# Optimization experiments

Measured on AMD Instinct MI355X. Metric: run time of the kernel, lower is better.

The kernel has to match this reference:

```python
import jax, jax.numpy as jnp
import numpy as np

B, N, DIM = 4, 1024, 2048
H, HKV, D = 16, 4, 128          # n_heads, n_kv_heads, head_dim
CACHE = 3072                     # cached KV length
WINDOW = 2048                    # max_window_len (sliding window)
EPS = 1e-6


def setup_inputs() -> dict:
    key = jax.random.key(0)
    ks = jax.random.split(key, 10)
    x = jax.random.normal(ks[0], (B, N, DIM), dtype=jnp.float32)
    past_k = jax.random.normal(ks[1], (B, HKV, CACHE, D), dtype=jnp.float32)
    past_v = jax.random.normal(ks[2], (B, HKV, CACHE, D), dtype=jnp.float32)
    # RoPE angles for the current segment (absolute positions CACHE..CACHE+N-1),
    # matching MultiLevelRoPE 'face' level: freqs = 1/theta**(arange(0,D,2)/D)
    pos = jnp.arange(CACHE, CACHE + N, dtype=jnp.float32)
    inv_freq = 1.0 / (10000.0 ** (jnp.arange(0, D, 2, dtype=jnp.float32) / D))
    ang = pos[:, None] * inv_freq[None, :]          # [N, D//2]
    freqs_cos = jnp.cos(ang)
    freqs_sin = jnp.sin(ang)
    s = 0.02
    Wq = jax.random.normal(ks[3], (H * D, DIM), dtype=jnp.float32) * s
    Wk = jax.random.normal(ks[4], (HKV * D, DIM), dtype=jnp.float32) * s
    Wv = jax.random.normal(ks[5], (HKV * D, DIM), dtype=jnp.float32) * s
    Wo = jax.random.normal(ks[6], (DIM, H * D), dtype=jnp.float32) * s
    bo = jnp.zeros((DIM,), dtype=jnp.float32)
    wq_norm = jnp.ones((D,), dtype=jnp.float32)
    wk_norm = jnp.ones((D,), dtype=jnp.float32)
    return {"x": x, "past_k": past_k, "past_v": past_v,
            "freqs_cos": freqs_cos, "freqs_sin": freqs_sin,
            "Wq": Wq, "Wk": Wk, "Wv": Wv, "Wo": Wo, "bo": bo,
            "wq_norm": wq_norm, "wk_norm": wk_norm}


def _rms_norm(t, w):
    # torch.nn.RMSNorm over head_dim
    return t * jax.lax.rsqrt(jnp.mean(t * t, axis=-1, keepdims=True) + EPS) * w


def _rope(t, cos, sin):
    # interleaved-pair complex rotation, as in MultiLevelRoPE.apply
    # t: [B, h, N, D]; cos/sin: [N, D//2]
    t2 = t.reshape(*t.shape[:-1], D // 2, 2)
    x0, x1 = t2[..., 0], t2[..., 1]
    c = cos[None, None, :, :]
    s = sin[None, None, :, :]
    r0 = x0 * c - x1 * s
    r1 = x0 * s + x1 * c
    return jnp.stack([r0, r1], axis=-1).reshape(t.shape)


def reference(x, past_k, past_v, freqs_cos, freqs_sin,
              Wq, Wk, Wv, Wo, bo, wq_norm, wk_norm):
    # projections -> [B, h, N, D]
    q = (x @ Wq.T).reshape(B, N, H, D).transpose(0, 2, 1, 3)
    k = (x @ Wk.T).reshape(B, N, HKV, D).transpose(0, 2, 1, 3)
    v = (x @ Wv.T).reshape(B, N, HKV, D).transpose(0, 2, 1, 3)
    # qk rms_norm on head_dim
    q = _rms_norm(q, wq_norm)
    k = _rms_norm(k, wk_norm)
    # RoPE on current segment (cached K already rotated)
    q = _rope(q, freqs_cos, freqs_sin)
    k = _rope(k, freqs_cos, freqs_sin)
    # append to cache -> M = CACHE + N
    k_all = jnp.concatenate([past_k, k], axis=2)   # [B, HKV, M, D]
    v_all = jnp.concatenate([past_v, v], axis=2)
    # repeat_kv for GQA
    n_rep = H // HKV
    k_rep = jnp.repeat(k_all, n_rep, axis=1)       # [B, H, M, D]
    v_rep = jnp.repeat(v_all, n_rep, axis=1)
    M = CACHE + N
    scale = 1.0 / jnp.sqrt(jnp.asarray(D, dtype=q.dtype))
    scores = jnp.einsum('bhnd,bhmd->bhnm', q, k_rep) * scale
    # causal + sliding-window mask over absolute positions
    qpos = jnp.arange(N) + CACHE                   # [N]
    kpos = jnp.arange(M)                           # [M]
    allowed = (kpos[None, :] <= qpos[:, None]) & (qpos[:, None] - kpos[None, :] < WINDOW)
    scores = jnp.where(allowed[None, None], scores, jnp.asarray(-1e30, dtype=scores.dtype))
    probs = jax.nn.softmax(scores, axis=-1)
    attn = jnp.einsum('bhnm,bhmd->bhnd', probs, v_rep)
    attn = attn.transpose(0, 2, 1, 3).reshape(B, N, H * D)
    return attn @ Wo.T + bo
```

## Files before the change

### kernel.cpp

```cpp
#include <hip/hip_runtime.h>
#include <hip/hip_bf16.h>
#include <stdint.h>

typedef unsigned short u16;
typedef unsigned int u32;
typedef __attribute__((ext_vector_type(8))) __bf16 bfrag;
typedef __attribute__((ext_vector_type(4))) float f32x4;
typedef __attribute__((ext_vector_type(4))) unsigned short u16x4;

__device__ __forceinline__ u16 f2bf(float f){
  union { float f; u32 u; } v; v.f = f;
  u32 u = v.u;
  return (u16)((u + 0x7fffu + ((u >> 16) & 1u)) >> 16);
}

__device__ __forceinline__ void gload_lds16(const void* g, void* l){
  __builtin_amdgcn_global_load_lds(
      (__attribute__((address_space(1))) void*)(unsigned long long)g,
      (__attribute__((address_space(3))) void*)(u32)(unsigned long long)l,
      16, 0, 0);
}

__global__ void __launch_bounds__(256) k_cvt(const float* __restrict__ s, u16* __restrict__ d, int n4){
  int i = blockIdx.x*256 + threadIdx.x;
  if (i >= n4) return;
  float4 v = ((const float4*)s)[i];
  u16x4 o; o[0]=f2bf(v.x); o[1]=f2bf(v.y); o[2]=f2bf(v.z); o[3]=f2bf(v.w);
  ((u16x4*)d)[i] = o;
}

__global__ void __launch_bounds__(256) k_cvt_past(const float* __restrict__ s, u16* __restrict__ d, int n4){
  int i = blockIdx.x*256 + threadIdx.x;
  if (i >= n4) return;
  int e = i*4;
  int row = e >> 7;
  int col = e & 127;
  int bh = row / 3072;
  int m = row - bh*3072;
  float4 v = ((const float4*)s)[i];
  u16x4 o; o[0]=f2bf(v.x); o[1]=f2bf(v.y); o[2]=f2bf(v.z); o[3]=f2bf(v.w);
  *(u16x4*)(d + ((size_t)(bh*4096 + m) << 7) + col) = o;
}

template<int EPI>
__global__ void __launch_bounds__(256) k_gemm(
    const u16* __restrict__ A, const u16* __restrict__ Bm,
    u16* __restrict__ Cb, float* __restrict__ Cf, const float* __restrict__ bias,
    int M, int Nn, int K)
{
  __shared__ u16 lsA[2][4096];
  __shared__ u16 lsB[2][4096];
  const int t = threadIdx.x, lane = t & 63, wid = t >> 6;
  const int l15 = lane & 15, l4 = lane >> 4;
  const int wm = wid >> 1, wn = wid & 1;
  const int bn = blockIdx.x, bm = blockIdx.y;
  const u16* Ab = A + (size_t)bm*128*K;
  const u16* Bb = Bm + (size_t)bn*128*K;

  auto stage = [&](u16* ls, const u16* g, int kof){
    #pragma unroll
    for (int r = 0; r < 2; ++r){
      int row = r*64 + (t >> 2);
      int s = (t & 3) ^ ((row >> 1) & 3);
      gload_lds16(g + (size_t)row*K + kof + s*8, ls + r*2048 + wid*512);
    }
  };

  f32x4 acc[4][4] = {};
  stage(&lsA[0][0], Ab, 0);
  stage(&lsB[0][0], Bb, 0);
  const int NT = K >> 5;
  const int sl = l4 ^ ((l15 >> 1) & 3);
  const int ra0 = wm*64 + l15, rb0 = wn*64 + l15;
  for (int kt = 0; kt < NT; ++kt){
    __syncthreads();
    const int cur = kt & 1;
    if (kt + 1 < NT){
      stage(&lsA[cur ^ 1][0], Ab, (kt + 1)*32);
      stage(&lsB[cur ^ 1][0], Bb, (kt + 1)*32);
    }
    bfrag af[4], bfv[4];
    #pragma unroll
    for (int i = 0; i < 4; ++i){
      af[i]  = *(const bfrag*)&lsA[cur][(ra0 + i*16)*32 + sl*8];
      bfv[i] = *(const bfrag*)&lsB[cur][(rb0 + i*16)*32 + sl*8];
    }
    #pragma unroll
    for (int i = 0; i < 4; ++i)
      #pragma unroll
      for (int j = 0; j < 4; ++j)
        acc[i][j] = __builtin_amdgcn_mfma_f32_16x16x32_bf16(af[i], bfv[j], acc[i][j], 0, 0, 0);
  }
  const int row0 = bm*128 + wm*64, col0 = bn*128 + wn*64;
  #pragma unroll
  for (int i = 0; i < 4; ++i)
    #pragma unroll
    for (int j = 0; j < 4; ++j){
      int cc = col0 + j*16 + l15;
      float bv = (EPI == 1) ? bias[cc] : 0.f;
      #pragma unroll
      for (int r = 0; r < 4; ++r){
        int rr = row0 + i*16 + l4*4 + r;
        if (EPI == 0) Cb[(size_t)rr*Nn + cc] = f2bf(acc[i][j][r]);
        else          Cf[(size_t)rr*Nn + cc] = acc[i][j][r] + bv;
      }
    }
}

__global__ void __launch_bounds__(256) k_rmsrope(
    const u16* __restrict__ proj, const float* __restrict__ cosb, const float* __restrict__ sinb,
    const float* __restrict__ wq, const float* __restrict__ wk,
    u16* __restrict__ q_ro, u16* __restrict__ k_all, u16* __restrict__ v_all)
{
  const int bn = blockIdx.x;
  const int b = bn >> 10, n = bn & 1023;
  const int lane = threadIdx.x & 63, w = threadIdx.x >> 6;
  const int chunk = blockIdx.y*4 + w;
  const u16* src = proj + (size_t)bn*3072 + chunk*128 + lane*2;
  const u32 raw = *(const u32*)src;
  union { u32 u; float f; } a, c2;
  a.u = raw << 16; c2.u = raw & 0xffff0000u;
  float x0 = a.f, x1 = c2.f;
  if (chunk >= 20){
    int hk = chunk - 20;
    *(u32*)(v_all + (((size_t)(b*4 + hk)*4096 + 3072 + n) << 7) + lane*2) = raw;
    return;
  }
  float ss = x0*x0 + x1*x1;
  #pragma unroll
  for (int m = 1; m < 64; m <<= 1) ss += __shfl_xor(ss, m, 64);
  float inv = rsqrtf(ss*(1.f/128.f) + 1e-6f);
  const float* wn2 = (chunk < 16) ? wq : wk;
  x0 *= inv*wn2[lane*2]; x1 *= inv*wn2[lane*2 + 1];
  float cz = cosb[n*64 + lane], sz = sinb[n*64 + lane];
  float r0 = x0*cz - x1*sz;
  float r1 = x0*sz + x1*cz;
  u32 outp = (u32)f2bf(r0) | ((u32)f2bf(r1) << 16);
  if (chunk < 16){
    *(u32*)(q_ro + (((size_t)(b*16 + chunk)*1024 + n) << 7) + lane*2) = outp;
  } else {
    int hk = chunk - 16;
    *(u32*)(k_all + (((size_t)(b*4 + hk)*4096 + 3072 + n) << 7) + lane*2) = outp;
  }
}

__global__ void __launch_bounds__(256) k_transpose_v(const u16* __restrict__ v_all, u16* __restrict__ v_t){
  __shared__ u16 T[64][65];
  const int mt = blockIdx.x, dt = blockIdx.y, pl = blockIdx.z;
  const u16* src = v_all + (size_t)pl*4096*128 + (size_t)mt*64*128 + dt*64;
  u16* dst = v_t + (size_t)pl*128*4096 + (size_t)dt*64*4096 + mt*64;
  const int t = threadIdx.x;
  #pragma unroll
  for (int r = 0; r < 2; ++r){
    int row = r*32 + (t >> 3);
    int c8 = (t & 7)*8;
    bfrag v = *(const bfrag*)(src + (size_t)row*128 + c8);
    union { bfrag v; u16 e[8]; } uv; uv.v = v;
    #pragma unroll
    for (int j = 0; j < 8; ++j) T[row][c8 + j] = uv.e[j];
  }
  __syncthreads();
  #pragma unroll
  for (int r = 0; r < 2; ++r){
    int drow = r*32 + (t >> 3);
    int m8 = (t & 7)*8;
    union { bfrag v; u16 e[8]; } uv;
    #pragma unroll
    for (int j = 0; j < 8; ++j) uv.e[j] = T[m8 + j][drow];
    *(bfrag*)(dst + (size_t)drow*4096 + m8) = uv.v;
  }
}

__global__ void __launch_bounds__(512) k_attn(
    const u16* __restrict__ q_ro, const u16* __restrict__ k_all,
    const u16* __restrict__ v_t, u16* __restrict__ attn_o)
{
  __shared__ u16 Kl[2][64*128];
  __shared__ u16 Vt[2][128*64];
  const int bid = blockIdx.x;
  const int qt = bid & 15, hk = (bid >> 4) & 3, b = bid >> 6;
  const int t = threadIdx.x, lane = t & 63, w = t >> 6;
  const int l15 = lane & 15, l4 = lane >> 4;
  const int h = hk*4 + (w >> 1);
  const int qbase = qt*64 + (w & 1)*32;

  const u16* qplane = q_ro + (size_t)(b*16 + h)*1024*128;
  const u16* kplane = k_all + (size_t)(b*4 + hk)*4096*128;
  const u16* vplane = v_t  + (size_t)(b*4 + hk)*128*4096;

  bfrag qf[2][4];
  #pragma unroll
  for (int qmi = 0; qmi < 2; ++qmi){
    const u16* qrow = qplane + (size_t)(qbase + qmi*16 + l15)*128;
    #pragma unroll
    for (int dks = 0; dks < 4; ++dks)
      qf[qmi][dks] = *(const bfrag*)(qrow + dks*32 + l4*8);
  }

  const int kb0 = qt*64 + 1024;
  auto stage = [&](int buf, int kb){
    #pragma unroll
    for (int r = 0; r < 2; ++r){
      int row = r*32 + (t >> 4);
      int s = (t & 15) ^ (row & 7);
      gload_lds16(kplane + (size_t)(kb + row)*128 + s*8, &Kl[buf][r*4096 + w*512]);
    }
    #pragma unroll
    for (int r = 0; r < 2; ++r){
      int row = r*64 + (t >> 3);
      int s = (t & 7) ^ (row & 7);
      gload_lds16(vplane + (size_t)row*4096 + kb + s*8, &Vt[buf][r*4096 + w*512]);
    }
  };

  f32x4 acc_o[8][2] = {};
  float m_run[2] = {-1e30f, -1e30f};
  float l_run[2] = {0.f, 0.f};
  const int qpos0 = 3072 + qbase + l15;
  const int qpmin = 3072 + qbase;
  const float sc = 0.08838834764831845f;

  stage(0, kb0);
  int cur = 0;
  for (int c = 0; c < 33; ++c){
    __syncthreads();
    const int kb = kb0 + c*64;
    if (c < 32) stage(cur ^ 1, kb + 64);

    f32x4 acc_s[4][2] = {};
    #pragma unroll
    for (int dks = 0; dks < 4; ++dks){
      bfrag kf[4];
      #pragma unroll
      for (int kni = 0; kni < 4; ++kni){
        int rk = kni*16 + l15;
        int slot = (dks*4 + l4) ^ (rk & 7);
        kf[kni] = *(const bfrag*)&Kl[cur][rk*128 + slot*8];
      }
      #pragma unroll
      for (int kni = 0; kni < 4; ++kni)
        #pragma unroll
        for (int qmi = 0; qmi < 2; ++qmi)
          acc_s[kni][qmi] = __builtin_amdgcn_mfma_f32_16x16x32_bf16(kf[kni], qf[qmi][dks], acc_s[kni][qmi], 0, 0, 0);
    }

    const bool full = (kb >= qpmin - 2016) && (kb + 63 <= qpmin);
    #pragma unroll
    for (int kni = 0; kni < 4; ++kni)
      #pragma unroll
      for (int qmi = 0; qmi < 2; ++qmi)
        #pragma unroll
        for (int r = 0; r < 4; ++r){
          float s = acc_s[kni][qmi][r]*sc;
          if (!full){
            int kpos = kb + kni*16 + l4*4 + r;
            int dq = (qpos0 + qmi*16) - kpos;
            if (dq < 0 || dq >= 2048) s = -__builtin_inff();
          }
          acc_s[kni][qmi][r] = s;
        }

    float ef[2];
    #pragma unroll
    for (int qmi = 0; qmi < 2; ++qmi){
      float mx = -__builtin_inff();
      #pragma unroll
      for (int kni = 0; kni < 4; ++kni)
        #pragma unroll
        for (int r = 0; r < 4; ++r) mx = fmaxf(mx, acc_s[kni][qmi][r]);
      mx = fmaxf(mx, __shfl_xor(mx, 16, 64));
      mx = fmaxf(mx, __shfl_xor(mx, 32, 64));
      float mnew = fmaxf(m_run[qmi], mx);
      ef[qmi] = __expf(m_run[qmi] - mnew);
      float ls = 0.f;
      #pragma unroll
      for (int kni = 0; kni < 4; ++kni)
        #pragma unroll
        for (int r = 0; r < 4; ++r){
          float p = __expf(acc_s[kni][qmi][r] - mnew);
          acc_s[kni][qmi][r] = p;
          ls += p;
        }
      ls += __shfl_xor(ls, 16, 64);
      ls += __shfl_xor(ls, 32, 64);
      l_run[qmi] = l_run[qmi]*ef[qmi] + ls;
      m_run[qmi] = mnew;
    }

    #pragma unroll
    for (int dj = 0; dj < 8; ++dj)
      #pragma unroll
      for (int qmi = 0; qmi < 2; ++qmi)
        #pragma unroll
        for (int r = 0; r < 4; ++r) acc_o[dj][qmi][r] *= ef[qmi];

    u32 pk[4][2][2];
    #pragma unroll
    for (int kni = 0; kni < 4; ++kni)
      #pragma unroll
      for (int qmi = 0; qmi < 2; ++qmi){
        pk[kni][qmi][0] = (u32)f2bf(acc_s[kni][qmi][0]) | ((u32)f2bf(acc_s[kni][qmi][1]) << 16);
        pk[kni][qmi][1] = (u32)f2bf(acc_s[kni][qmi][2]) | ((u32)f2bf(acc_s[kni][qmi][3]) << 16);
      }

    const int srcA = ((l4 & 1) << 5) + l15;
    const int srcB = srcA + 16;
    const bool hi = (l4 >> 1) != 0;
    #pragma unroll
    for (int ks = 0; ks < 2; ++ks){
      bfrag vf[8];
      #pragma unroll
      for (int dj = 0; dj < 8; ++dj){
        int rd = dj*16 + l15;
        int slot = (ks*4 + l4) ^ (rd & 7);
        vf[dj] = *(const bfrag*)&Vt[cur][rd*64 + slot*8];
      }
      #pragma unroll
      for (int qmi = 0; qmi < 2; ++qmi){
        u32 a0 = (u32)__shfl((int)pk[ks*2][qmi][0], srcA, 64);
        u32 a1 = (u32)__shfl((int)pk[ks*2][qmi][1], srcA, 64);
        u32 b0 = (u32)__shfl((int)pk[ks*2][qmi][0], srcB, 64);
        u32 b1 = (u32)__shfl((int)pk[ks*2][qmi][1], srcB, 64);
        u32 c0 = (u32)__shfl((int)pk[ks*2+1][qmi][0], srcA, 64);
        u32 c1 = (u32)__shfl((int)pk[ks*2+1][qmi][1], srcA, 64);
        u32 d0 = (u32)__shfl((int)pk[ks*2+1][qmi][0], srcB, 64);
        u32 d1 = (u32)__shfl((int)pk[ks*2+1][qmi][1], srcB, 64);
        union { u32 u[4]; bfrag v; } pf;
        pf.u[0] = hi ? c0 : a0;
        pf.u[1] = hi ? c1 : a1;
        pf.u[2] = hi ? d0 : b0;
        pf.u[3] = hi ? d1 : b1;
        #pragma unroll
        for (int dj = 0; dj < 8; ++dj)
          acc_o[dj][qmi] = __builtin_amdgcn_mfma_f32_16x16x32_bf16(vf[dj], pf.v, acc_o[dj][qmi], 0, 0, 0);
      }
    }
    cur ^= 1;
  }

  #pragma unroll
  for (int qmi = 0; qmi < 2; ++qmi){
    float inv = 1.0f / l_run[qmi];
    int bn = b*1024 + qbase + qmi*16 + l15;
    u16* orow = attn_o + (size_t)bn*2048 + h*128;
    #pragma unroll
    for (int dj = 0; dj < 8; ++dj){
      u16x4 o;
      #pragma unroll
      for (int r = 0; r < 4; ++r) o[r] = f2bf(acc_o[dj][qmi][r]*inv);
      *(u16x4*)(orow + dj*16 + l4*4) = o;
    }
  }
}

extern "C" void kernel_launch(void* const* d_in, const int* in_sizes, int n_in,
                              void* d_out, int out_size, void* d_ws, size_t ws_size,
                              hipStream_t stream)
{
  const float* x      = (const float*)d_in[0];
  const float* past_k = (const float*)d_in[1];
  const float* past_v = (const float*)d_in[2];
  const float* fcos   = (const float*)d_in[3];
  const float* fsin   = (const float*)d_in[4];
  const float* Wq     = (const float*)d_in[5];
  const float* Wk     = (const float*)d_in[6];
  const float* Wv     = (const float*)d_in[7];
  const float* Wo     = (const float*)d_in[8];
  const float* bo     = (const float*)d_in[9];
  const float* wqn    = (const float*)d_in[10];
  const float* wkn    = (const float*)d_in[11];
  float* out = (float*)d_out;
  char* ws = (char*)d_ws;

  u16* xb    = (u16*)(ws);
  u16* wqkv  = (u16*)(ws + 16777216);
  u16* wo_b  = (u16*)(ws + 29360128);
  u16* q_ro  = (u16*)(ws + 37748736);
  u16* k_all = (u16*)(ws + 54525952);
  u16* v_all = (u16*)(ws + 71303168);
  u16* v_t   = (u16*)(ws + 88080384);
  u16* proj  = (u16*)(ws + 104857600);
  u16* attn_o = proj;

  k_cvt<<<8192, 256, 0, stream>>>(x, xb, 2097152);
  k_cvt<<<4096, 256, 0, stream>>>(Wq, wqkv, 1048576);
  k_cvt<<<1024, 256, 0, stream>>>(Wk, wqkv + 2048*2048, 262144);
  k_cvt<<<1024, 256, 0, stream>>>(Wv, wqkv + 2560*2048, 262144);
  k_cvt<<<4096, 256, 0, stream>>>(Wo, wo_b, 1048576);
  k_cvt_past<<<6144, 256, 0, stream>>>(past_k, k_all, 1572864);
  k_cvt_past<<<6144, 256, 0, stream>>>(past_v, v_all, 1572864);

  k_gemm<0><<<dim3(24, 32), 256, 0, stream>>>(xb, wqkv, proj, nullptr, nullptr, 4096, 3072, 2048);
  k_rmsrope<<<dim3(4096, 6), 256, 0, stream>>>(proj, fcos, fsin, wqn, wkn, q_ro, k_all, v_all);
  k_transpose_v<<<dim3(64, 2, 16), 256, 0, stream>>>(v_all, v_t);
  k_attn<<<256, 512, 0, stream>>>(q_ro, k_all, v_t, attn_o);
  k_gemm<1><<<dim3(16, 32), 256, 0, stream>>>(attn_o, wo_b, nullptr, out, bo, 4096, 2048, 2048);
}
```

Before: 285.5 us.

## Rewrite attention with 32x32 MFMA, lazy rescale, and fuse past-V conversion with transpose

```diff
diff --git a/kernel.cpp b/kernel.cpp
--- a/kernel.cpp
+++ b/kernel.cpp
@@ -6,12 +6,20 @@
 typedef unsigned int u32;
 typedef __attribute__((ext_vector_type(8))) __bf16 bfrag;
 typedef __attribute__((ext_vector_type(4))) float f32x4;
+typedef __attribute__((ext_vector_type(16))) float f32x16;
 typedef __attribute__((ext_vector_type(4))) unsigned short u16x4;
 
 __device__ __forceinline__ u16 f2bf(float f){
   union { float f; u32 u; } v; v.f = f;
   u32 u = v.u;
   return (u16)((u + 0x7fffu + ((u >> 16) & 1u)) >> 16);
+}
+
+__device__ __forceinline__ u32 cvtpk(float a, float b){
+  u32 r; asm("v_cvt_pk_bf16_f32 %0, %1, %2" : "=v"(r) : "v"(a), "v"(b)); return r;
+}
+__device__ __forceinline__ void swap32(u32 &a, u32 &b){
+  asm volatile("v_permlane32_swap_b32 %0, %1" : "+v"(a), "+v"(b));
 }
 
 __device__ __forceinline__ void gload_lds16(const void* g, void* l){
@@ -40,6 +48,33 @@
   float4 v = ((const float4*)s)[i];
   u16x4 o; o[0]=f2bf(v.x); o[1]=f2bf(v.y); o[2]=f2bf(v.z); o[3]=f2bf(v.w);
   *(u16x4*)(d + ((size_t)(bh*4096 + m) << 7) + col) = o;
+}
+
+__global__ void __launch_bounds__(256) k_cvt_past_vt(const float* __restrict__ s, u16* __restrict__ v_t){
+  __shared__ u16 T[64][65];
+  const int mt = blockIdx.x, dt = blockIdx.y, pl = blockIdx.z;
+  const float* src = s + (size_t)pl*3072*128 + (size_t)mt*64*128 + dt*64;
+  u16* dst = v_t + (size_t)pl*128*4096 + (size_t)dt*64*4096 + mt*64;
+  const int t = threadIdx.x;
+  #pragma unroll
+  for (int r = 0; r < 2; ++r){
+    int row = r*32 + (t >> 3);
+    int c8 = (t & 7)*8;
+    float4 va = *(const float4*)(src + (size_t)row*128 + c8);
+    float4 vb = *(const float4*)(src + (size_t)row*128 + c8 + 4);
+    T[row][c8+0]=f2bf(va.x); T[row][c8+1]=f2bf(va.y); T[row][c8+2]=f2bf(va.z); T[row][c8+3]=f2bf(va.w);
+    T[row][c8+4]=f2bf(vb.x); T[row][c8+5]=f2bf(vb.y); T[row][c8+6]=f2bf(vb.z); T[row][c8+7]=f2bf(vb.w);
+  }
+  __syncthreads();
+  #pragma unroll
+  for (int r = 0; r < 2; ++r){
+    int drow = r*32 + (t >> 3);
+    int m8 = (t & 7)*8;
+    union { bfrag v; u16 e[8]; } uv;
+    #pragma unroll
+    for (int j = 0; j < 8; ++j) uv.e[j] = T[m8 + j][drow];
+    *(bfrag*)(dst + (size_t)drow*4096 + m8) = uv.v;
+  }
 }
 
 template<int EPI>
@@ -146,7 +181,7 @@
 
 __global__ void __launch_bounds__(256) k_transpose_v(const u16* __restrict__ v_all, u16* __restrict__ v_t){
   __shared__ u16 T[64][65];
-  const int mt = blockIdx.x, dt = blockIdx.y, pl = blockIdx.z;
+  const int mt = blockIdx.x + 48, dt = blockIdx.y, pl = blockIdx.z;
   const u16* src = v_all + (size_t)pl*4096*128 + (size_t)mt*64*128 + dt*64;
   u16* dst = v_t + (size_t)pl*128*4096 + (size_t)dt*64*4096 + mt*64;
   const int t = threadIdx.x;
@@ -171,54 +206,54 @@
   }
 }
 
-__global__ void __launch_bounds__(512) k_attn(
+__global__ void __launch_bounds__(256, 2) k_attn(
     const u16* __restrict__ q_ro, const u16* __restrict__ k_all,
     const u16* __restrict__ v_t, u16* __restrict__ attn_o)
 {
   __shared__ u16 Kl[2][64*128];
   __shared__ u16 Vt[2][128*64];
   const int bid = blockIdx.x;
-  const int qt = bid & 15, hk = (bid >> 4) & 3, b = bid >> 6;
+  const int xcd = bid & 7, idx = bid >> 3;
+  const int plane = (xcd << 1) | (idx >> 5);
+  const int qt = idx & 31;
+  const int b = plane >> 2, hk = plane & 3;
   const int t = threadIdx.x, lane = t & 63, w = t >> 6;
-  const int l15 = lane & 15, l4 = lane >> 4;
-  const int h = hk*4 + (w >> 1);
-  const int qbase = qt*64 + (w & 1)*32;
+  const int l31 = lane & 31, lh = lane >> 5;
+  const int h = hk*4 + w;
+  const int qbase = qt*32;
 
   const u16* qplane = q_ro + (size_t)(b*16 + h)*1024*128;
   const u16* kplane = k_all + (size_t)(b*4 + hk)*4096*128;
   const u16* vplane = v_t  + (size_t)(b*4 + hk)*128*4096;
 
-  bfrag qf[2][4];
-  #pragma unroll
-  for (int qmi = 0; qmi < 2; ++qmi){
-    const u16* qrow = qplane + (size_t)(qbase + qmi*16 + l15)*128;
-    #pragma unroll
-    for (int dks = 0; dks < 4; ++dks)
-      qf[qmi][dks] = *(const bfrag*)(qrow + dks*32 + l4*8);
-  }
-
-  const int kb0 = qt*64 + 1024;
+  bfrag qf[8];
+  {
+    const u16* qrow = qplane + (size_t)(qbase + l31)*128 + lh*8;
+    #pragma unroll
+    for (int dks = 0; dks < 8; ++dks)
+      qf[dks] = *(const bfrag*)(qrow + dks*16);
+  }
+
   auto stage = [&](int buf, int kb){
     #pragma unroll
-    for (int r = 0; r < 2; ++r){
-      int row = r*32 + (t >> 4);
-      int s = (t & 15) ^ (row & 7);
-      gload_lds16(kplane + (size_t)(kb + row)*128 + s*8, &Kl[buf][r*4096 + w*512]);
-    }
-    #pragma unroll
-    for (int r = 0; r < 2; ++r){
-      int row = r*64 + (t >> 3);
-      int s = (t & 7) ^ (row & 7);
-      gload_lds16(vplane + (size_t)row*4096 + kb + s*8, &Vt[buf][r*4096 + w*512]);
+    for (int r = 0; r < 4; ++r){
+      int row = r*16 + (t >> 4);
+      int scol = ((t & 15) ^ (row & 7) ^ ((row & 8) ? 8 : 0) ^ ((row & 8) ? 8 : 0)) * 8;
+      gload_lds16(kplane + (size_t)(kb + row)*128 + (((t & 15) ^ (row & 7))*8), &Kl[buf][r*2048 + t*8]);
+      (void)scol;
+    }
+    #pragma unroll
+    for (int r = 0; r < 4; ++r){
+      int row = r*32 + (t >> 3);
+      gload_lds16(vplane + (size_t)row*4096 + kb + (((t & 7) ^ (row & 7))*8), &Vt[buf][r*2048 + t*8]);
     }
   };
 
-  f32x4 acc_o[8][2] = {};
-  float m_run[2] = {-1e30f, -1e30f};
-  float l_run[2] = {0.f, 0.f};
-  const int qpos0 = 3072 + qbase + l15;
-  const int qpmin = 3072 + qbase;
-  const float sc = 0.08838834764831845f;
+  f32x16 acc_o[4] = {};
+  float m_run = -1e30f, l_run = 0.f;
+  const float KL = 0.127529904f;
+  const int kb0 = (qbase + 1024) & ~63;
+  const int qpos = 3072 + qbase + l31;
 
   stage(0, kb0);
   int cur = 0;
@@ -227,130 +262,99 @@
     const int kb = kb0 + c*64;
     if (c < 32) stage(cur ^ 1, kb + 64);
 
-    f32x4 acc_s[4][2] = {};
-    #pragma unroll
-    for (int dks = 0; dks < 4; ++dks){
-      bfrag kf[4];
-      #pragma unroll
-      for (int kni = 0; kni < 4; ++kni){
-        int rk = kni*16 + l15;
-        int slot = (dks*4 + l4) ^ (rk & 7);
-        kf[kni] = *(const bfrag*)&Kl[cur][rk*128 + slot*8];
+    f32x16 s0 = {}, s1 = {};
+    #pragma unroll
+    for (int dks = 0; dks < 8; ++dks){
+      const int sw = l31 & 7;
+      bfrag k0 = *(const bfrag*)&Kl[cur][(l31)*128      + (((dks*2 + lh) ^ sw)*8)];
+      bfrag k1 = *(const bfrag*)&Kl[cur][(32 + l31)*128 + (((dks*2 + lh) ^ sw)*8)];
+      s0 = __builtin_amdgcn_mfma_f32_32x32x16_bf16(k0, qf[dks], s0, 0, 0, 0);
+      s1 = __builtin_amdgcn_mfma_f32_32x32x16_bf16(k1, qf[dks], s1, 0, 0, 0);
+    }
+
+    if ((c == 0) | (c == 32)){
+      #pragma unroll
+      for (int r = 0; r < 16; ++r){
+        int krow = (r & 3) + 8*(r >> 2) + 4*lh;
+        int d0 = qpos - (kb + krow);
+        int d1 = qpos - (kb + 32 + krow);
+        if ((unsigned)d0 >= 2048u) s0[r] = -1e30f;
+        if ((unsigned)d1 >= 2048u) s1[r] = -1e30f;
       }
-      #pragma unroll
-      for (int kni = 0; kni < 4; ++kni)
+    }
+
+    float mx = s0[0];
+    #pragma unroll
+    for (int r = 1; r < 16; ++r) mx = fmaxf(mx, s0[r]);
+    #pragma unroll
+    for (int r = 0; r < 16; ++r) mx = fmaxf(mx, s1[r]);
+    mx = fmaxf(mx, __shfl_xor(mx, 32, 64));
+
+    if (__any(mx > m_run + 62.7f)){
+      float mnew = fmaxf(m_run, mx);
+      float ef = exp2f(KL*(m_run - mnew));
+      m_run = mnew;
+      l_run *= ef;
+      #pragma unroll
+      for (int dj = 0; dj < 4; ++dj)
         #pragma unroll
-        for (int qmi = 0; qmi < 2; ++qmi)
-          acc_s[kni][qmi] = __builtin_amdgcn_mfma_f32_16x16x32_bf16(kf[kni], qf[qmi][dks], acc_s[kni][qmi], 0, 0, 0);
-    }
-
-    const bool full = (kb >= qpmin - 2016) && (kb + 63 <= qpmin);
-    #pragma unroll
-    for (int kni = 0; kni < 4; ++kni)
-      #pragma unroll
-      for (int qmi = 0; qmi < 2; ++qmi)
-        #pragma unroll
-        for (int r = 0; r < 4; ++r){
-          float s = acc_s[kni][qmi][r]*sc;
-          if (!full){
-            int kpos = kb + kni*16 + l4*4 + r;
-            int dq = (qpos0 + qmi*16) - kpos;
-            if (dq < 0 || dq >= 2048) s = -__builtin_inff();
-          }
-          acc_s[kni][qmi][r] = s;
-        }
-
-    float ef[2];
-    #pragma unroll
-    for (int qmi = 0; qmi < 2; ++qmi){
-      float mx = -__builtin_inff();
-      #pragma unroll
-      for (int kni = 0; kni < 4; ++kni)
-        #pragma unroll
-        for (int r = 0; r < 4; ++r) mx = fmaxf(mx, acc_s[kni][qmi][r]);
-      mx = fmaxf(mx, __shfl_xor(mx, 16, 64));
-      mx = fmaxf(mx, __shfl_xor(mx, 32, 64));
-      float mnew = fmaxf(m_run[qmi], mx);
-      ef[qmi] = __expf(m_run[qmi] - mnew);
-      float ls = 0.f;
-      #pragma unroll
-      for (int kni = 0; kni < 4; ++kni)
-        #pragma unroll
-        for (int r = 0; r < 4; ++r){
-          float p = __expf(acc_s[kni][qmi][r] - mnew);
-          acc_s[kni][qmi][r] = p;
-          ls += p;
-        }
-      ls += __shfl_xor(ls, 16, 64);
-      ls += __shfl_xor(ls, 32, 64);
-      l_run[qmi] = l_run[qmi]*ef[qmi] + ls;
-      m_run[qmi] = mnew;
-    }
-
-    #pragma unroll
-    for (int dj = 0; dj < 8; ++dj)
-      #pragma unroll
-      for (int qmi = 0; qmi < 2; ++qmi)
-        #pragma unroll
-        for (int r = 0; r < 4; ++r) acc_o[dj][qmi][r] *= ef[qmi];
-
-    u32 pk[4][2][2];
-    #pragma unroll
-    for (int kni = 0; kni < 4; ++kni)
-      #pragma unroll
-      for (int qmi = 0; qmi < 2; ++qmi){
-        pk[kni][qmi][0] = (u32)f2bf(acc_s[kni][qmi][0]) | ((u32)f2bf(acc_s[kni][qmi][1]) << 16);
-        pk[kni][qmi][1] = (u32)f2bf(acc_s[kni][qmi][2]) | ((u32)f2bf(acc_s[kni][qmi][3]) << 16);
+        for (int r = 0; r < 16; ++r) acc_o[dj][r] *= ef;
+    }
+    const float nKm = -KL*m_run;
+    float ls = 0.f;
+    #pragma unroll
+    for (int r = 0; r < 16; ++r){ float p = exp2f(fmaf(KL, s0[r], nKm)); s0[r] = p; ls += p; }
+    #pragma unroll
+    for (int r = 0; r < 16; ++r){ float p = exp2f(fmaf(KL, s1[r], nKm)); s1[r] = p; ls += p; }
+    l_run += ls;
+
+    union { u32 u[4]; bfrag v; } pfrag[4];
+    {
+      u32 a0 = cvtpk(s0[0],  s0[1]),  a1 = cvtpk(s0[2],  s0[3]);
+      u32 b0 = cvtpk(s0[4],  s0[5]),  b1 = cvtpk(s0[6],  s0[7]);
+      swap32(a0, b0); swap32(a1, b1);
+      pfrag[0].u[0]=a0; pfrag[0].u[1]=a1; pfrag[0].u[2]=b0; pfrag[0].u[3]=b1;
+      u32 c0 = cvtpk(s0[8],  s0[9]),  c1 = cvtpk(s0[10], s0[11]);
+      u32 e0 = cvtpk(s0[12], s0[13]), e1 = cvtpk(s0[14], s0[15]);
+      swap32(c0, e0); swap32(c1, e1);
+      pfrag[1].u[0]=c0; pfrag[1].u[1]=c1; pfrag[1].u[2]=e0; pfrag[1].u[3]=e1;
+    }
+    {
+      u32 a0 = cvtpk(s1[0],  s1[1]),  a1 = cvtpk(s1[2],  s1[3]);
+      u32 b0 = cvtpk(s1[4],  s1[5]),  b1 = cvtpk(s1[6],  s1[7]);
+      swap32(a0, b0); swap32(a1, b1);
+      pfrag[2].u[0]=a0; pfrag[2].u[1]=a1; pfrag[2].u[2]=b0; pfrag[2].u[3]=b1;
+      u32 c0 = cvtpk(s1[8],  s1[9]),  c1 = cvtpk(s1[10], s1[11]);
+      u32 e0 = cvtpk(s1[12], s1[13]), e1 = cvtpk(s1[14], s1[15]);
+      swap32(c0, e0); swap32(c1, e1);
+      pfrag[3].u[0]=c0; pfrag[3].u[1]=c1; pfrag[3].u[2]=e0; pfrag[3].u[3]=e1;
+    }
+
+    #pragma unroll
+    for (int ks = 0; ks < 4; ++ks)
+      #pragma unroll
+      for (int dj = 0; dj < 4; ++dj){
+        int row = dj*32 + l31;
+        bfrag vf = *(const bfrag*)&Vt[cur][row*64 + (((ks*2 + lh) ^ (row & 7))*8)];
+        acc_o[dj] = __builtin_amdgcn_mfma_f32_32x32x16_bf16(vf, pfrag[ks].v, acc_o[dj], 0, 0, 0);
       }
-
-    const int srcA = ((l4 & 1) << 5) + l15;
-    const int srcB = srcA + 16;
-    const bool hi = (l4 >> 1) != 0;
-    #pragma unroll
-    for (int ks = 0; ks < 2; ++ks){
-      bfrag vf[8];
-      #pragma unroll
-      for (int dj = 0; dj < 8; ++dj){
-        int rd = dj*16 + l15;
-        int slot = (ks*4 + l4) ^ (rd & 7);
-        vf[dj] = *(const bfrag*)&Vt[cur][rd*64 + slot*8];
-      }
-      #pragma unroll
-      for (int qmi = 0; qmi < 2; ++qmi){
-        u32 a0 = (u32)__shfl((int)pk[ks*2][qmi][0], srcA, 64);
-        u32 a1 = (u32)__shfl((int)pk[ks*2][qmi][1], srcA, 64);
-        u32 b0 = (u32)__shfl((int)pk[ks*2][qmi][0], srcB, 64);
-        u32 b1 = (u32)__shfl((int)pk[ks*2][qmi][1], srcB, 64);
-        u32 c0 = (u32)__shfl((int)pk[ks*2+1][qmi][0], srcA, 64);
-        u32 c1 = (u32)__shfl((int)pk[ks*2+1][qmi][1], srcA, 64);
-        u32 d0 = (u32)__shfl((int)pk[ks*2+1][qmi][0], srcB, 64);
-        u32 d1 = (u32)__shfl((int)pk[ks*2+1][qmi][1], srcB, 64);
-        union { u32 u[4]; bfrag v; } pf;
-        pf.u[0] = hi ? c0 : a0;
-        pf.u[1] = hi ? c1 : a1;
-        pf.u[2] = hi ? d0 : b0;
-        pf.u[3] = hi ? d1 : b1;
-        #pragma unroll
-        for (int dj = 0; dj < 8; ++dj)
-          acc_o[dj][qmi] = __builtin_amdgcn_mfma_f32_16x16x32_bf16(vf[dj], pf.v, acc_o[dj][qmi], 0, 0, 0);
-      }
-    }
     cur ^= 1;
   }
 
-  #pragma unroll
-  for (int qmi = 0; qmi < 2; ++qmi){
-    float inv = 1.0f / l_run[qmi];
-    int bn = b*1024 + qbase + qmi*16 + l15;
-    u16* orow = attn_o + (size_t)bn*2048 + h*128;
-    #pragma unroll
-    for (int dj = 0; dj < 8; ++dj){
+  float lt = l_run + __shfl_xor(l_run, 32, 64);
+  float inv = 1.0f / lt;
+  const int bn = b*1024 + qbase + l31;
+  u16* orow = attn_o + (size_t)bn*2048 + h*128;
+  #pragma unroll
+  for (int dj = 0; dj < 4; ++dj)
+    #pragma unroll
+    for (int rg = 0; rg < 4; ++rg){
+      int d0 = dj*32 + rg*8 + 4*lh;
       u16x4 o;
       #pragma unroll
-      for (int r = 0; r < 4; ++r) o[r] = f2bf(acc_o[dj][qmi][r]*inv);
-      *(u16x4*)(orow + dj*16 + l4*4) = o;
-    }
-  }
+      for (int r2 = 0; r2 < 4; ++r2) o[r2] = f2bf(acc_o[dj][rg*4 + r2]*inv);
+      *(u16x4*)(orow + d0) = o;
+    }
 }
 
 extern "C" void kernel_launch(void* const* d_in, const int* in_sizes, int n_in,
@@ -388,11 +392,11 @@
   k_cvt<<<1024, 256, 0, stream>>>(Wv, wqkv + 2560*2048, 262144);
   k_cvt<<<4096, 256, 0, stream>>>(Wo, wo_b, 1048576);
   k_cvt_past<<<6144, 256, 0, stream>>>(past_k, k_all, 1572864);
-  k_cvt_past<<<6144, 256, 0, stream>>>(past_v, v_all, 1572864);
+  k_cvt_past_vt<<<dim3(48, 2, 16), 256, 0, stream>>>(past_v, v_t);
 
   k_gemm<0><<<dim3(24, 32), 256, 0, stream>>>(xb, wqkv, proj, nullptr, nullptr, 4096, 3072, 2048);
   k_rmsrope<<<dim3(4096, 6), 256, 0, stream>>>(proj, fcos, fsin, wqn, wkn, q_ro, k_all, v_all);
-  k_transpose_v<<<dim3(64, 2, 16), 256, 0, stream>>>(v_all, v_t);
-  k_attn<<<256, 512, 0, stream>>>(q_ro, k_all, v_t, attn_o);
+  k_transpose_v<<<dim3(16, 2, 16), 256, 0, stream>>>(v_all, v_t);
+  k_attn<<<512, 256, 0, stream>>>(q_ro, k_all, v_t, attn_o);
   k_gemm<1><<<dim3(16, 32), 256, 0, stream>>>(attn_o, wo_b, nullptr, out, bo, 4096, 2048, 2048);
 }
```

New measurement: 257.4 us. 9.8% less time.
